# Performance work log

Measured on AMD Instinct MI355X. Metric: run time of the kernel, lower is better.

The kernel has to match this reference:

```python
import jax, jax.numpy as jnp
import numpy as np

B, S, E, H = 1, 8192, 1024, 16
D = E // H
SEG_LENS = [2048, 4096, 8192]
DILATIONS = [1, 2, 4]


def setup_inputs() -> dict:
    key = jax.random.key(0)
    k0, k1, k2 = jax.random.split(key, 3)
    sc_in = 1.0 / np.sqrt(E)
    return {
        "x": jax.random.normal(k0, (B, S, E), jnp.float32),
        "w_qkv": jax.random.normal(k1, (3 * E, E), jnp.float32) * sc_in,
        "b_qkv": jnp.zeros((3 * E,), jnp.float32),
        "w_out": jax.random.normal(k2, (E, E), jnp.float32) * sc_in,
        "b_out": jnp.zeros((E,), jnp.float32),
    }


def _sdpa(q, k, v):
    # q,k,v: [B,H,N,D]; standard scaled dot-product attention (non-causal)
    scale = 1.0 / np.sqrt(q.shape[-1])
    scores = jnp.einsum('bhqd,bhkd->bhqk', q, k) * scale
    probs = jax.nn.softmax(scores, axis=-1)
    return jnp.einsum('bhqk,bhkd->bhqd', probs, v)


def reference(x, w_qkv, b_qkv, w_out, b_out):
    # QKV projection: torch Linear is x @ W^T + b
    qkv = x @ w_qkv.T + b_qkv                       # [B,S,3E]
    qkv = qkv.reshape(B, S, 3, H, D).transpose(2, 0, 3, 1, 4)  # [3,B,H,S,D]
    q, k, v = qkv[0], qkv[1], qkv[2]

    seg_outputs = []
    for seg_len, dil in zip(SEG_LENS, DILATIONS):
        if seg_len > S:
            continue
        if dil > 1:
            n = min(seg_len, S // dil)
            pos = np.arange(0, n * dil, dil)        # strided dilated gather
        else:
            pos = np.arange(seg_len)                # leading segment
        o = _sdpa(q[:, :, pos], k[:, :, pos], v[:, :, pos])
        # scatter back to full length (zero elsewhere); also handles zero-padding
        full = jnp.zeros((B, H, S, D), x.dtype).at[:, :, pos, :].set(o)
        seg_outputs.append(full)

    if len(seg_outputs) == 0:
        out = jnp.zeros((B, H, S, D), x.dtype)
    else:
        out = seg_outputs[0]
        for so in seg_outputs[1:]:
            out = out + so
        out = out / len(seg_outputs)                # stack(...).mean(0)

    out = out.transpose(0, 2, 1, 3).reshape(B, S, E)
    return out @ w_out.T + b_out
```

## Files before the change

### kernel.cpp

```cpp
#include <hip/hip_runtime.h>


typedef __attribute__((ext_vector_type(8))) short bf16x8;
typedef __attribute__((ext_vector_type(4))) float f32x4;

#define MFMA(a, b, c) __builtin_amdgcn_mfma_f32_16x16x32_bf16((a), (b), (c), 0, 0, 0)

#if __has_builtin(__builtin_amdgcn_exp2f)
#define EXP2(x) __builtin_amdgcn_exp2f(x)
#else
#define EXP2(x) exp2f(x)
#endif

static __device__ __forceinline__ unsigned short f2bf(float f) {
  unsigned int u = __float_as_uint(f);
  unsigned int r = (u + 0x7FFFu + ((u >> 16) & 1u)) >> 16;
  return (unsigned short)r;
}

__global__ void cvt_f32_bf16(const float* __restrict__ in,
                             unsigned short* __restrict__ out, int n8) {
  int i = blockIdx.x * blockDim.x + threadIdx.x;
  if (i >= n8) return;
  const float4* p = (const float4*)in + (size_t)i * 2;
  float4 a = p[0];
  float4 b = p[1];
  union { bf16x8 v; unsigned short u[8]; } o;
  o.u[0] = f2bf(a.x); o.u[1] = f2bf(a.y); o.u[2] = f2bf(a.z); o.u[3] = f2bf(a.w);
  o.u[4] = f2bf(b.x); o.u[5] = f2bf(b.y); o.u[6] = f2bf(b.z); o.u[7] = f2bf(b.w);
  *((bf16x8*)out + i) = o.v;
}

template <int EPILOGUE>
__global__ __launch_bounds__(256, 2) void gemm_bt(
    const unsigned short* __restrict__ A, const unsigned short* __restrict__ B,
    const float* __restrict__ bias, void* __restrict__ Cout, int N, int K) {
  __shared__ unsigned short At[128 * 32];
  __shared__ unsigned short Bt[128 * 32];
  const int tid = threadIdx.x;
  const int wave = tid >> 6, lane = tid & 63;
  const int quad = lane >> 4, lc = lane & 15;
  const int wm = (wave >> 1) * 64, wn = (wave & 1) * 64;
  const int m0 = blockIdx.x * 128, n0 = blockIdx.y * 128;

  f32x4 acc[4][4] = {};

  for (int k0 = 0; k0 < K; k0 += 32) {
    __syncthreads();
#pragma unroll
    for (int issue = 0; issue < 2; ++issue) {
      const int cbase = issue * 256 + wave * 64;
      const int c = cbase + lane;
      const int row = c >> 2, col8 = (c & 3) * 8;
      __builtin_amdgcn_global_load_lds(
          (const __attribute__((address_space(1))) void*)&A[(size_t)(m0 + row) * K + k0 + col8],
          (__attribute__((address_space(3))) void*)&At[cbase * 8], 16, 0, 0);
      __builtin_amdgcn_global_load_lds(
          (const __attribute__((address_space(1))) void*)&B[(size_t)(n0 + row) * K + k0 + col8],
          (__attribute__((address_space(3))) void*)&Bt[cbase * 8], 16, 0, 0);
    }
    __syncthreads();
    bf16x8 af[4], bfr[4];
#pragma unroll
    for (int t = 0; t < 4; ++t)
      af[t] = *(const bf16x8*)&At[(wm + t * 16 + lc) * 32 + quad * 8];
#pragma unroll
    for (int t = 0; t < 4; ++t)
      bfr[t] = *(const bf16x8*)&Bt[(wn + t * 16 + lc) * 32 + quad * 8];
#pragma unroll
    for (int i = 0; i < 4; ++i)
#pragma unroll
      for (int j = 0; j < 4; ++j)
        acc[i][j] = MFMA(af[i], bfr[j], acc[i][j]);
  }

#pragma unroll
  for (int i = 0; i < 4; ++i) {
#pragma unroll
    for (int j = 0; j < 4; ++j) {
      const int gcol = n0 + wn + j * 16 + lc;
      const float bs = bias[gcol];
#pragma unroll
      for (int r = 0; r < 4; ++r) {
        const int grow = m0 + wm + i * 16 + quad * 4 + r;
        const float v = acc[i][j][r] + bs;
        if (EPILOGUE == 0) {
          const int which = gcol >> 10, rem = gcol & 1023;
          const int hh = rem >> 6, d = rem & 63;
          const float vs = (which == 0) ? v * 0.18033688f : v;
          ((unsigned short*)Cout)[(((size_t)(which * 16 + hh)) * 8192 + grow) * 64 + d] = f2bf(vs);
        } else {
          ((float*)Cout)[(size_t)grow * N + gcol] = v;
        }
      }
    }
  }
}

__global__ void transpose_v(const unsigned short* __restrict__ v,
                            unsigned short* __restrict__ vt1,
                            unsigned short* __restrict__ vt2,
                            unsigned short* __restrict__ vt3) {
  __shared__ unsigned short Tt[64 * 72];
  const int tid = threadIdx.x;
  const int h = blockIdx.y;
  const int bx = blockIdx.x;
  const unsigned short* src = v + (size_t)h * 8192 * 64;
  unsigned short* dst;
  int dil, Nk, t0;
  if (bx < 32)      { dst = vt1; dil = 1; Nk = 2048; t0 = bx; }
  else if (bx < 96) { dst = vt2; dil = 2; Nk = 4096; t0 = bx - 32; }
  else              { dst = vt3; dil = 4; Nk = 2048; t0 = bx - 96; }
  dst += (size_t)h * 64 * Nk;
  const int j0 = t0 * 64;
#pragma unroll
  for (int it = 0; it < 2; ++it) {
    const int slot = tid + it * 256;
    const int jj = slot >> 3, c8 = (slot & 7) * 8;
    *(bf16x8*)&Tt[jj * 72 + c8] =
        *(const bf16x8*)&src[(size_t)(j0 + jj) * dil * 64 + c8];
  }
  __syncthreads();
  const int d = tid >> 2, pg = (tid & 3) * 16;
  union { bf16x8 v2[2]; unsigned short u[16]; } ob;
#pragma unroll
  for (int t = 0; t < 16; ++t) {
    const int pos = pg + t;
    const int w = pos & 31;
    const int jj = (pos & 32) | (((w >> 2) & 1) * 16 + (w >> 3) * 4 + (w & 3));
    ob.u[t] = Tt[jj * 72 + d];
  }
  *(bf16x8*)&dst[(size_t)d * Nk + j0 + pg] = ob.v2[0];
  *(bf16x8*)&dst[(size_t)d * Nk + j0 + pg + 8] = ob.v2[1];
}

__global__ __launch_bounds__(512, 2) void flash_all(
    const unsigned short* __restrict__ qkvb,
    const unsigned short* __restrict__ vt1, float* __restrict__ o1,
    const unsigned short* __restrict__ vt2, float* __restrict__ o2,
    const unsigned short* __restrict__ vt3, float* __restrict__ o3) {
  __shared__ unsigned short Smem[3 * 8192 + 128];

  const int bx = blockIdx.x;
  int z, h, qt;
  if ((bx & 1) == 0) { const int i = bx >> 1; z = 1; h = i >> 4; qt = i & 15; }
  else { const int j = bx >> 1; z = (j & 1) ? 2 : 0; const int i = j >> 1; h = i >> 3; qt = i & 7; }
  const int Nk = (z == 1) ? 4096 : 2048;
  const int dil = 1 << z;
  const unsigned short* vt = (z == 0) ? vt1 : (z == 1) ? vt2 : vt3;
  float* o = (z == 0) ? o1 : (z == 1) ? o2 : o3;

  const int tid = threadIdx.x;
  const int wave = tid >> 6, lane = tid & 63;
  const int quad = lane >> 4, lc = lane & 15;
  const int ks = wave >> 2, wq = wave & 3;

  const unsigned short* qh = qkvb + (size_t)h * 8192 * 64;
  const unsigned short* kh = qkvb + (size_t)(16 + h) * 8192 * 64;
  const unsigned short* vh = vt + (size_t)h * 64 * Nk;

  bf16x8 qf[4][2];
#pragma unroll
  for (int mb = 0; mb < 4; ++mb) {
    const size_t qrow = (size_t)(qt * 256 + wq * 64 + mb * 16 + lc) * dil;
    qf[mb][0] = *(const bf16x8*)&qh[qrow * 64 + quad * 8];
    qf[mb][1] = *(const bf16x8*)&qh[qrow * 64 + quad * 8 + 32];
  }

  union { bf16x8 v; unsigned short u[8]; } one_u;
#pragma unroll
  for (int t = 0; t < 8; ++t) one_u.u[t] = 0x3F80;
  const bf16x8 vone = one_u.v;

  f32x4 oacc[4][4] = {};
  f32x4 lacc[4] = {};

  const int srow = wave * 8 + (lane >> 3);
  const int kchunk = (lane & 7) ^ (srow & 7);
  const size_t kstep = (size_t)64 * dil * 64;
  const unsigned short* kp = &kh[(size_t)(srow * dil) * 64 + kchunk * 8];
  const unsigned short* vp = &vh[(size_t)srow * Nk + kchunk * 8];

#define STAGE(b)                                                               \
  do {                                                                         \
    __builtin_amdgcn_global_load_lds(                                          \
        (const __attribute__((address_space(1))) void*)kp,                     \
        (__attribute__((address_space(3))) void*)&Smem[(b) * 8192 + wave * 512], \
        16, 0, 0);                                                             \
    __builtin_amdgcn_global_load_lds(                                          \
        (const __attribute__((address_space(1))) void*)vp,                     \
        (__attribute__((address_space(3))) void*)&Smem[(b) * 8192 + 4096 + wave * 512], \
        16, 0, 0);                                                             \
    kp += kstep;                                                               \
    vp += 64;                                                                  \
  } while (0)

  const int NT = Nk >> 6;
  STAGE(0);
  STAGE(1);
  asm volatile("s_waitcnt vmcnt(2)" ::: "memory");
  __builtin_amdgcn_s_barrier();
  __builtin_amdgcn_sched_barrier(0);

  int bR = 0, bS = 2;
  for (int t = 0; t < NT; ++t) {
    if (t + 2 < NT) STAGE(bS);
    const unsigned short* Kt = &Smem[bR * 8192];
    const unsigned short* Vt = &Smem[bR * 8192 + 4096];

    union { unsigned int u[4]; bf16x8 v; } pb[4];
#pragma unroll
    for (int t2 = 0; t2 < 2; ++t2) {
      const int row = (ks * 2 + t2) * 16 + lc;
      const bf16x8 ka0 = *(const bf16x8*)&Kt[row * 64 + ((quad ^ (lc & 7)) * 8)];
      const bf16x8 ka1 = *(const bf16x8*)&Kt[row * 64 + (((4 + quad) ^ (lc & 7)) * 8)];
#pragma unroll
      for (int mb = 0; mb < 4; ++mb) {
        f32x4 zz = {};
        zz = MFMA(ka0, qf[mb][0], zz);
        zz = MFMA(ka1, qf[mb][1], zz);
        const float e0 = EXP2(zz[0]);
        const float e1 = EXP2(zz[1]);
        const float e2 = EXP2(zz[2]);
        const float e3 = EXP2(zz[3]);
        unsigned int p01, p23;
        asm("v_cvt_pk_bf16_f32 %0, %1, %2" : "=v"(p01) : "v"(e0), "v"(e1));
        asm("v_cvt_pk_bf16_f32 %0, %1, %2" : "=v"(p23) : "v"(e2), "v"(e3));
        pb[mb].u[t2 * 2 + 0] = p01;
        pb[mb].u[t2 * 2 + 1] = p23;
      }
    }

    __builtin_amdgcn_s_setprio(1);
#pragma unroll
    for (int nb = 0; nb < 4; ++nb) {
      const int vrow = nb * 16 + lc;
      const bf16x8 va = *(const bf16x8*)&Vt[vrow * 64 + (((ks * 4 + quad) ^ (lc & 7)) * 8)];
#pragma unroll
      for (int mb = 0; mb < 4; ++mb)
        oacc[mb][nb] = MFMA(va, pb[mb].v, oacc[mb][nb]);
    }
#pragma unroll
    for (int mb = 0; mb < 4; ++mb) lacc[mb] = MFMA(vone, pb[mb].v, lacc[mb]);
    __builtin_amdgcn_s_setprio(0);

    if (t + 1 < NT) {
      if (t + 2 < NT) asm volatile("s_waitcnt vmcnt(2)" ::: "memory");
      else            asm volatile("s_waitcnt vmcnt(0)" ::: "memory");
      __builtin_amdgcn_s_barrier();
      __builtin_amdgcn_sched_barrier(0);
    }
    bR = (bR == 2) ? 0 : bR + 1;
    bS = (bS == 2) ? 0 : bS + 1;
  }

  __syncthreads();
  float* Wo = (float*)Smem + wq * 16 * 64;
  float* Wp = (float*)Smem + 4096 + wq * 16 * 64;
  float* lbuf = (float*)Smem + 8192;
  const int g = lane >> 2, s4 = lane & 3;
#pragma unroll
  for (int mb = 0; mb < 4; ++mb) {
    if (wave >= 4) {
#pragma unroll
      for (int nb = 0; nb < 4; ++nb) {
        const int c = nb * 4 + quad;
        const int cs = (c & 8) | ((c & 7) ^ (lc & 7));
        *(f32x4*)&Wp[lc * 64 + cs * 4] = oacc[mb][nb];
      }
      if (quad == 0) lbuf[wq * 16 + lc] = lacc[mb][0];
    }
    __syncthreads();
    if (wave < 4) {
      const float inv = 1.0f / (3.0f * (lacc[mb][0] + lbuf[wq * 16 + lc]));
#pragma unroll
      for (int nb = 0; nb < 4; ++nb) {
        const int c = nb * 4 + quad;
        const int cs = (c & 8) | ((c & 7) ^ (lc & 7));
        f32x4 val = oacc[mb][nb] + *(const f32x4*)&Wp[lc * 64 + cs * 4];
        val *= inv;
        *(f32x4*)&Wo[lc * 64 + cs * 4] = val;
      }
      const size_t base = (size_t)(qt * 256 + wq * 64 + mb * 16 + g) * 1024 +
                          (size_t)h * 64 + s4 * 16;
#pragma unroll
      for (int c2 = 0; c2 < 4; ++c2) {
        const int c = s4 * 4 + c2;
        const int cs = (c & 8) | ((c & 7) ^ (g & 7));
        *(float4*)&o[base + c2 * 4] = *(const float4*)&Wo[g * 64 + cs * 4];
      }
    }
    __syncthreads();
  }
#undef STAGE
}

__global__ void combine(const float* __restrict__ o1, const float* __restrict__ o2,
                        const float* __restrict__ o3,
                        unsigned short* __restrict__ a3b) {
  const int idx = blockIdx.x * 256 + threadIdx.x;
  const int s = idx >> 7, e = (idx & 127) * 8;
  float acc[8] = {};
  if (s < 2048) {
    const float* p = &o1[(size_t)s * 1024 + e];
#pragma unroll
    for (int t = 0; t < 8; ++t) acc[t] += p[t];
  }
  if (!(s & 1)) {
    const float* p = &o2[(size_t)(s >> 1) * 1024 + e];
#pragma unroll
    for (int t = 0; t < 8; ++t) acc[t] += p[t];
  }
  if (!(s & 3)) {
    const float* p = &o3[(size_t)(s >> 2) * 1024 + e];
#pragma unroll
    for (int t = 0; t < 8; ++t) acc[t] += p[t];
  }
  union { bf16x8 v; unsigned short u[8]; } ob;
#pragma unroll
  for (int t = 0; t < 8; ++t) ob.u[t] = f2bf(acc[t]);
  *(bf16x8*)&a3b[(size_t)s * 1024 + e] = ob.v;
}

extern "C" void kernel_launch(void* const* d_in, const int* in_sizes, int n_in,
                              void* d_out, int out_size, void* d_ws, size_t ws_size,
                              hipStream_t stream) {
  const float* x     = (const float*)d_in[0];
  const float* w_qkv = (const float*)d_in[1];
  const float* b_qkv = (const float*)d_in[2];
  const float* w_out = (const float*)d_in[3];
  const float* b_out = (const float*)d_in[4];
  float* out = (float*)d_out;

  char* ws = (char*)d_ws;
  unsigned short* qkvb  = (unsigned short*)(ws);
  float*          o1    = (float*)(ws + 33554432);
  float*          o3    = (float*)(ws + 41943040);
  unsigned short* vt1   = (unsigned short*)(ws + 50331648);
  unsigned short* vt2   = (unsigned short*)(ws + 54525952);
  unsigned short* vt3   = (unsigned short*)(ws + 62914560);
  float*          o2    = (float*)(ws + 67108864);
  unsigned short* wqkvb = (unsigned short*)(ws + 83886080);
  unsigned short* woutb = (unsigned short*)(ws + 90177536);
  unsigned short* xb    = (unsigned short*)(ws + 92274688);
  unsigned short* a3b   = xb;

  cvt_f32_bf16<<<dim3(8388608 / 8 / 256), dim3(256), 0, stream>>>(x, xb, 8388608 / 8);
  cvt_f32_bf16<<<dim3(3145728 / 8 / 256), dim3(256), 0, stream>>>(w_qkv, wqkvb, 3145728 / 8);
  cvt_f32_bf16<<<dim3(1048576 / 8 / 256), dim3(256), 0, stream>>>(w_out, woutb, 1048576 / 8);

  gemm_bt<0><<<dim3(64, 24), dim3(256), 0, stream>>>(xb, wqkvb, b_qkv, qkvb, 3072, 1024);

  transpose_v<<<dim3(128, 16), dim3(256), 0, stream>>>(qkvb + (size_t)32 * 8192 * 64,
                                                       vt1, vt2, vt3);

  flash_all<<<dim3(512), dim3(512), 0, stream>>>(qkvb, vt1, o1, vt2, o2, vt3, o3);

  combine<<<dim3(4096), dim3(256), 0, stream>>>(o1, o2, o3, a3b);

  gemm_bt<1><<<dim3(64, 8), dim3(256), 0, stream>>>(a3b, woutb, b_out, out, 1024, 1024);
}
```

Baseline: 347.0 us.

## Load K/V fragments directly from global into registers, dropping LDS staging

Replaces the triple-buffered global_load_lds pipeline of K and V tiles, with its waitcnt and barriers, by direct per-lane global loads of the MFMA fragments into registers. This removes LDS traffic and block-wide barriers from the inner loop. Shared memory now serves only the epilogue reduction. In exchange there is no explicit prefetch, so latency hiding depends on the compiler and occupancy, and each wave loads its own K/V slices (8 of 16-byte pieces per lane per step). The V loads are strided by Nk rows and rely on caching.

```diff
diff --git a/kernel.cpp b/kernel.cpp
--- a/kernel.cpp
+++ b/kernel.cpp
@@ -139,7 +139,7 @@
     const unsigned short* __restrict__ vt1, float* __restrict__ o1,
     const unsigned short* __restrict__ vt2, float* __restrict__ o2,
     const unsigned short* __restrict__ vt3, float* __restrict__ o3) {
-  __shared__ unsigned short Smem[3 * 8192 + 128];
+  __shared__ float Sep[8192 + 64];
 
   const int bx = blockIdx.x;
   int z, h, qt;
@@ -175,50 +175,31 @@
   f32x4 oacc[4][4] = {};
   f32x4 lacc[4] = {};
 
-  const int srow = wave * 8 + (lane >> 3);
-  const int kchunk = (lane & 7) ^ (srow & 7);
+  const unsigned short* kp0 = kh + (size_t)((ks * 32 + lc) * dil) * 64 + quad * 8;
+  const unsigned short* kp1 = kh + (size_t)((ks * 32 + 16 + lc) * dil) * 64 + quad * 8;
+  const unsigned short* vp = vh + (size_t)lc * Nk + (ks * 4 + quad) * 8;
   const size_t kstep = (size_t)64 * dil * 64;
-  const unsigned short* kp = &kh[(size_t)(srow * dil) * 64 + kchunk * 8];
-  const unsigned short* vp = &vh[(size_t)srow * Nk + kchunk * 8];
-
-#define STAGE(b)                                                               \
-  do {                                                                         \
-    __builtin_amdgcn_global_load_lds(                                          \
-        (const __attribute__((address_space(1))) void*)kp,                     \
-        (__attribute__((address_space(3))) void*)&Smem[(b) * 8192 + wave * 512], \
-        16, 0, 0);                                                             \
-    __builtin_amdgcn_global_load_lds(                                          \
-        (const __attribute__((address_space(1))) void*)vp,                     \
-        (__attribute__((address_space(3))) void*)&Smem[(b) * 8192 + 4096 + wave * 512], \
-        16, 0, 0);                                                             \
-    kp += kstep;                                                               \
-    vp += 64;                                                                  \
-  } while (0)
-
-  const int NT = Nk >> 6;
-  STAGE(0);
-  STAGE(1);
-  asm volatile("s_waitcnt vmcnt(2)" ::: "memory");
-  __builtin_amdgcn_s_barrier();
-  __builtin_amdgcn_sched_barrier(0);
-
-  int bR = 0, bS = 2;
-  for (int t = 0; t < NT; ++t) {
-    if (t + 2 < NT) STAGE(bS);
-    const unsigned short* Kt = &Smem[bR * 8192];
-    const unsigned short* Vt = &Smem[bR * 8192 + 4096];
+
+  for (int kb = 0; kb < Nk; kb += 64) {
+    bf16x8 ka[2][2], va[4];
+    ka[0][0] = *(const bf16x8*)(kp0);
+    ka[0][1] = *(const bf16x8*)(kp0 + 32);
+    ka[1][0] = *(const bf16x8*)(kp1);
+    ka[1][1] = *(const bf16x8*)(kp1 + 32);
+    va[0] = *(const bf16x8*)(vp);
+    va[1] = *(const bf16x8*)(vp + (size_t)16 * Nk);
+    va[2] = *(const bf16x8*)(vp + (size_t)32 * Nk);
+    va[3] = *(const bf16x8*)(vp + (size_t)48 * Nk);
+    kp0 += kstep; kp1 += kstep; vp += 64;
 
     union { unsigned int u[4]; bf16x8 v; } pb[4];
 #pragma unroll
     for (int t2 = 0; t2 < 2; ++t2) {
-      const int row = (ks * 2 + t2) * 16 + lc;
-      const bf16x8 ka0 = *(const bf16x8*)&Kt[row * 64 + ((quad ^ (lc & 7)) * 8)];
-      const bf16x8 ka1 = *(const bf16x8*)&Kt[row * 64 + (((4 + quad) ^ (lc & 7)) * 8)];
 #pragma unroll
       for (int mb = 0; mb < 4; ++mb) {
         f32x4 zz = {};
-        zz = MFMA(ka0, qf[mb][0], zz);
-        zz = MFMA(ka1, qf[mb][1], zz);
+        zz = MFMA(ka[t2][0], qf[mb][0], zz);
+        zz = MFMA(ka[t2][1], qf[mb][1], zz);
         const float e0 = EXP2(zz[0]);
         const float e1 = EXP2(zz[1]);
         const float e2 = EXP2(zz[2]);
@@ -234,30 +215,18 @@
     __builtin_amdgcn_s_setprio(1);
 #pragma unroll
     for (int nb = 0; nb < 4; ++nb) {
-      const int vrow = nb * 16 + lc;
-      const bf16x8 va = *(const bf16x8*)&Vt[vrow * 64 + (((ks * 4 + quad) ^ (lc & 7)) * 8)];
 #pragma unroll
       for (int mb = 0; mb < 4; ++mb)
-        oacc[mb][nb] = MFMA(va, pb[mb].v, oacc[mb][nb]);
+        oacc[mb][nb] = MFMA(va[nb], pb[mb].v, oacc[mb][nb]);
     }
 #pragma unroll
     for (int mb = 0; mb < 4; ++mb) lacc[mb] = MFMA(vone, pb[mb].v, lacc[mb]);
     __builtin_amdgcn_s_setprio(0);
-
-    if (t + 1 < NT) {
-      if (t + 2 < NT) asm volatile("s_waitcnt vmcnt(2)" ::: "memory");
-      else            asm volatile("s_waitcnt vmcnt(0)" ::: "memory");
-      __builtin_amdgcn_s_barrier();
-      __builtin_amdgcn_sched_barrier(0);
-    }
-    bR = (bR == 2) ? 0 : bR + 1;
-    bS = (bS == 2) ? 0 : bS + 1;
-  }
-
-  __syncthreads();
-  float* Wo = (float*)Smem + wq * 16 * 64;
-  float* Wp = (float*)Smem + 4096 + wq * 16 * 64;
-  float* lbuf = (float*)Smem + 8192;
+  }
+
+  float* Wo = Sep + wq * 16 * 64;
+  float* Wp = Sep + 4096 + wq * 16 * 64;
+  float* lbuf = Sep + 8192;
   const int g = lane >> 2, s4 = lane & 3;
 #pragma unroll
   for (int mb = 0; mb < 4; ++mb) {
@@ -292,7 +261,6 @@
     }
     __syncthreads();
   }
-#undef STAGE
 }
 
 __global__ void combine(const float* __restrict__ o1, const float* __restrict__ o2,
```

Measured after the change: 443.6 us. +27.8%, slower.
